# Performance work log

Measured on AMD Instinct MI355X. Metric: run time of the kernel, lower is better.

Reference implementation:

```python
import jax, jax.numpy as jnp
import numpy as np

B, S, D, H = 16, 2048, 1024, 1024

def setup_inputs() -> dict:
    key = jax.random.key(0)
    k1, k2, k3 = jax.random.split(key, 3)
    X = jax.random.normal(k1, (B, S, D), dtype=jnp.float32)
    W = jax.random.normal(k2, (3 * H, D), dtype=jnp.float32) * (1.0 / np.sqrt(D))
    b = jax.random.normal(k3, (3 * H,), dtype=jnp.float32) * 0.01
    return {"X": X, "W": W, "b": b}

def forget_mult(z, f):
    # z, f: [B, S, H]; h_t = z_t * f_t + (1 - f_t) * h_{t-1}, h_{-1} = 0
    z_t = jnp.moveaxis(z, 1, 0)  # [S, B, H]
    f_t = jnp.moveaxis(f, 1, 0)
    h0 = jnp.zeros(z.shape[::2], dtype=z.dtype)  # [B, H]
    def step(h, zf):
        zt, ft = zf
        h = zt * ft + (1.0 - ft) * h
        return h, h
    _, cs = jax.lax.scan(step, h0, (z_t, f_t))
    return jnp.moveaxis(cs, 0, 1)  # [B, S, H]

def reference(X, W, b):
    # window=1, output_gate=True, batch_first=True, zoneout=0, hidden=None
    Y = jnp.einsum('bsd,ed->bse', X, W) + b  # [B, S, 3H]
    z_gate, f_gate, o_gate = jnp.split(Y, 3, axis=2)
    z_gate = jnp.tanh(z_gate)
    f_gate = jax.nn.sigmoid(f_gate)
    c_gate = forget_mult(z_gate, f_gate)
    output = jax.nn.sigmoid(o_gate) * c_gate
    return output, c_gate[:, -1:]
```

## Files before the change

kernel.cpp:

```cpp
#include <hip/hip_runtime.h>
#include <hip/hip_bf16.h>
#include <hip/hip_fp16.h>


#define BB 16
#define SS 2048
#define DD 1024
#define HH 1024
#define N3 3072
#define CHUNK 64
#define NC (SS/CHUNK)

#define BM 256
#define BN 256
#define BK 64
#define NKT (DD/BK)

typedef _Float16 f16x8 __attribute__((ext_vector_type(8)));
typedef float    f32x4 __attribute__((ext_vector_type(4)));

__device__ __forceinline__ float sigm_f(float x) {
    return 1.0f / (1.0f + __expf(-x));
}
__device__ __forceinline__ float tanh_f(float x) {
    float ax = fabsf(x);
    float e  = __expf(2.0f * ax);
    float r  = 1.0f - 2.0f / (e + 1.0f);
    return copysignf(r, x);
}

__global__ __launch_bounds__(256) void cvt_f32_f16(
    const float* __restrict__ src, __half* __restrict__ dst, int n8)
{
    int i = blockIdx.x * 256 + threadIdx.x;
    if (i >= n8) return;
    const float4* s = (const float4*)src + (size_t)i * 2;
    float4 a = s[0], b = s[1];
    f16x8 v;
    v[0] = (_Float16)a.x; v[1] = (_Float16)a.y; v[2] = (_Float16)a.z; v[3] = (_Float16)a.w;
    v[4] = (_Float16)b.x; v[5] = (_Float16)b.y; v[6] = (_Float16)b.z; v[7] = (_Float16)b.w;
    *((f16x8*)dst + i) = v;
}

__global__ __launch_bounds__(512) void gemm_gates8(
    const __half* __restrict__ Xs,
    const __half* __restrict__ W16,
    const float*  __restrict__ bias,
    __half* __restrict__ G)
{
    __shared__ __half As[2][BM * BK] __attribute__((aligned(16)));
    __shared__ __half Bs[2][BN * BK] __attribute__((aligned(16)));

    const int t   = threadIdx.x;
    const int wid = t >> 6;
    const int l   = t & 63;
    const int m0  = blockIdx.x * BM;
    const int n0  = blockIdx.y * BN;
    const int wr  = wid >> 2;
    const int wc  = wid & 3;
    const int cl  = l & 15;
    const int kg  = l >> 4;
    const int cs  = cl & 7;

    f32x4 acc[8][4];
    #pragma unroll
    for (int m = 0; m < 8; ++m)
        #pragma unroll
        for (int n = 0; n < 4; ++n)
            acc[m][n] = f32x4{0.f, 0.f, 0.f, 0.f};

    const int srow = wid * 8 + (l >> 3);
    const int scol = (((l & 7) ^ ((l >> 3) & 7)) * 8);
    const __half* Xb = Xs  + (size_t)(m0 + srow) * DD + scol;
    const __half* Wb = W16 + (size_t)(n0 + srow) * DD + scol;

#define ISSUE_A(slot, j, kt) \
    __builtin_amdgcn_global_load_lds( \
        (const __attribute__((address_space(1))) void*)(Xb + (size_t)(j) * 64 * DD + (kt) * BK), \
        (__attribute__((address_space(3))) void*)(&As[slot][(j) * 4096 + wid * 512]), 16, 0, 0)
#define ISSUE_B(slot, j, kt) \
    __builtin_amdgcn_global_load_lds( \
        (const __attribute__((address_space(1))) void*)(Wb + (size_t)(j) * 64 * DD + (kt) * BK), \
        (__attribute__((address_space(3))) void*)(&Bs[slot][(j) * 4096 + wid * 512]), 16, 0, 0)

#define READ_A(rh) \
    _Pragma("unroll") \
    for (int i = 0; i < 4; ++i) \
        _Pragma("unroll") \
        for (int kh = 0; kh < 2; ++kh) \
            a[i][kh] = *(const f16x8*)(Ab + ((wr * 128 + ((rh) * 4 + i) * 16 + cl) * BK \
                                             + (((kh * 4 + kg) ^ cs) * 8)))
#define READ_B(bd, ch) \
    _Pragma("unroll") \
    for (int j = 0; j < 2; ++j) \
        _Pragma("unroll") \
        for (int kh = 0; kh < 2; ++kh) \
            bd[j][kh] = *(const f16x8*)(Bb + ((wc * 64 + ((ch) * 2 + j) * 16 + cl) * BK \
                                              + (((kh * 4 + kg) ^ cs) * 8)))

#define MFMA_Q(rh, ch, bd) \
    __builtin_amdgcn_s_barrier(); \
    asm volatile("s_waitcnt lgkmcnt(0)" ::: "memory"); \
    __builtin_amdgcn_sched_barrier(0); \
    __builtin_amdgcn_s_setprio(1); \
    _Pragma("unroll") \
    for (int kh = 0; kh < 2; ++kh) \
        _Pragma("unroll") \
        for (int i = 0; i < 4; ++i) \
            _Pragma("unroll") \
            for (int j = 0; j < 2; ++j) \
                acc[(rh) * 4 + i][(ch) * 2 + j] = __builtin_amdgcn_mfma_f32_16x16x32_f16( \
                    a[i][kh], bd[j][kh], acc[(rh) * 4 + i][(ch) * 2 + j], 0, 0, 0); \
    __builtin_amdgcn_s_setprio(0); \
    __builtin_amdgcn_sched_barrier(0); \
    __builtin_amdgcn_s_barrier()

    ISSUE_A(0, 0, 0); ISSUE_A(0, 1, 0); ISSUE_A(0, 2, 0); ISSUE_A(0, 3, 0);
    ISSUE_B(0, 0, 0); ISSUE_B(0, 1, 0); ISSUE_B(0, 2, 0); ISSUE_B(0, 3, 0);

    for (int kt = 0; kt < NKT; ++kt) {
        const int cur = kt & 1, nxt = cur ^ 1;
        const __half* Ab = As[cur];
        const __half* Bb = Bs[cur];

        if (kt + 1 < NKT) {
            ISSUE_A(nxt, 0, kt + 1); ISSUE_A(nxt, 1, kt + 1);
            ISSUE_A(nxt, 2, kt + 1); ISSUE_A(nxt, 3, kt + 1);
            asm volatile("s_waitcnt vmcnt(4)" ::: "memory");
        } else {
            asm volatile("s_waitcnt vmcnt(0)" ::: "memory");
        }
        __builtin_amdgcn_s_barrier();

        f16x8 a[4][2], b0[2][2], b1[2][2];

        READ_A(0); READ_B(b0, 0);
        MFMA_Q(0, 0, b0);

        READ_B(b1, 1);
        if (kt + 1 < NKT) {
            ISSUE_B(nxt, 0, kt + 1); ISSUE_B(nxt, 1, kt + 1);
            ISSUE_B(nxt, 2, kt + 1); ISSUE_B(nxt, 3, kt + 1);
        }
        MFMA_Q(0, 1, b1);

        READ_A(1);
        MFMA_Q(1, 1, b1);

        MFMA_Q(1, 0, b0);
    }
#undef MFMA_Q
#undef READ_A
#undef READ_B
#undef ISSUE_A
#undef ISSUE_B

    #pragma unroll
    for (int fc = 0; fc < 4; ++fc) {
        const int gcol = n0 + wc * 64 + fc * 16 + cl;
        const float bv = bias[gcol];
        #pragma unroll
        for (int fr = 0; fr < 8; ++fr) {
            const int grow0 = m0 + wr * 128 + fr * 16 + kg * 4;
            #pragma unroll
            for (int i = 0; i < 4; ++i) {
                G[(size_t)(grow0 + i) * N3 + gcol] = __float2half(acc[fr][fc][i] + bv);
            }
        }
    }
}

__global__ __launch_bounds__(256) void scan_pass1(
    const __half* __restrict__ G,
    float* __restrict__ Ac, float* __restrict__ Fc)
{
    const int flat = blockIdx.x * 256 + threadIdx.x;
    const int h  = flat & (HH - 1);
    const int c  = (flat >> 10) & (NC - 1);
    const int lb = flat >> 15;

    const __half* g = G + (size_t)(lb * SS + c * CHUNK) * N3 + h;
    float A = 0.f, F = 1.f;
    for (int s = 0; s < CHUNK; ++s) {
        float z = __half2float(g[0]);
        float f = __half2float(g[HH]);
        g += N3;
        float ft = sigm_f(f);
        float fp = 1.f - ft;
        A = tanh_f(z) * ft + fp * A;
        F *= fp;
    }
    Ac[flat] = A;
    Fc[flat] = F;
}

__global__ __launch_bounds__(256) void scan_pass2(
    const float* __restrict__ Ac, const float* __restrict__ Fc,
    float* __restrict__ Hin, float* __restrict__ c_last)
{
    const int flat = blockIdx.x * 256 + threadIdx.x;
    const int lb = flat >> 10;
    const int h  = flat & (HH - 1);
    float hc = 0.f;
    for (int c = 0; c < NC; ++c) {
        const size_t idx = (size_t)(lb * NC + c) * HH + h;
        Hin[idx] = hc;
        hc = Ac[idx] + Fc[idx] * hc;
    }
    c_last[flat] = hc;
}

__global__ __launch_bounds__(256) void scan_pass3(
    const __half* __restrict__ G, const float* __restrict__ Hin,
    float* __restrict__ out)
{
    const int flat = blockIdx.x * 256 + threadIdx.x;
    const int h  = flat & (HH - 1);
    const int c  = (flat >> 10) & (NC - 1);
    const int lb = flat >> 15;

    const __half* g = G + (size_t)(lb * SS + c * CHUNK) * N3 + h;
    float* o = out + (size_t)(lb * SS + c * CHUNK) * HH + h;
    float hc = Hin[flat];
    for (int s = 0; s < CHUNK; ++s) {
        float z  = __half2float(g[0]);
        float f  = __half2float(g[HH]);
        float og = __half2float(g[2 * HH]);
        g += N3;
        float ft = sigm_f(f);
        hc = tanh_f(z) * ft + (1.f - ft) * hc;
        *o = hc * sigm_f(og);
        o += HH;
    }
}

extern "C" void kernel_launch(void* const* d_in, const int* in_sizes, int n_in,
                              void* d_out, int out_size, void* d_ws, size_t ws_size,
                              hipStream_t stream) {
    const float* X    = (const float*)d_in[0];
    const float* W    = (const float*)d_in[1];
    const float* bias = (const float*)d_in[2];
    for (int i = 0; i < n_in && i < 3; ++i) {
        if      (in_sizes[i] == BB * SS * DD) X    = (const float*)d_in[i];
        else if (in_sizes[i] == N3 * DD)      W    = (const float*)d_in[i];
        else if (in_sizes[i] == N3)           bias = (const float*)d_in[i];
    }
    float* out = (float*)d_out;
    float* c_last_base = out + (size_t)BB * SS * HH;

    const size_t w16_b   = (size_t)N3 * DD * sizeof(__half);
    const size_t per_b_x = (size_t)SS * DD * sizeof(__half);
    const size_t per_b_g = (size_t)SS * N3 * sizeof(__half);
    const size_t per_b_s = (size_t)NC * HH * sizeof(float) * 3;
    int nb = 1;
    for (int cand = BB; cand >= 1; --cand) {
        if (w16_b + (size_t)cand * (per_b_x + per_b_g + per_b_s) <= ws_size) {
            nb = cand; break;
        }
    }

    __half* W16 = (__half*)d_ws;
    __half* X16 = (__half*)((char*)W16 + w16_b);
    __half* G   = (__half*)((char*)X16 + (size_t)nb * per_b_x);
    float*  Ac  = (float*)((char*)G + (size_t)nb * per_b_g);
    float*  Fc  = Ac + (size_t)nb * NC * HH;
    float*  Hin = Fc + (size_t)nb * NC * HH;

    {
        const int n8 = (N3 * DD) / 8;
        cvt_f32_f16<<<(n8 + 255) / 256, 256, 0, stream>>>(W, W16, n8);
    }

    for (int b0 = 0; b0 < BB; b0 += nb) {
        const int bs = (b0 + nb <= BB) ? nb : (BB - b0);

        const int n8x = (bs * SS * DD) / 8;
        cvt_f32_f16<<<(n8x + 255) / 256, 256, 0, stream>>>(
            X + (size_t)b0 * SS * DD, X16, n8x);

        dim3 gg(bs * (SS / BM), N3 / BN);
        gemm_gates8<<<gg, 512, 0, stream>>>(X16, W16, bias, G);

        scan_pass1<<<(bs * NC * HH) / 256, 256, 0, stream>>>(G, Ac, Fc);
        scan_pass2<<<(bs * HH) / 256, 256, 0, stream>>>(Ac, Fc, Hin,
                                                        c_last_base + (size_t)b0 * HH);
        scan_pass3<<<(bs * NC * HH) / 256, 256, 0, stream>>>(G, Hin,
                                                             out + (size_t)b0 * SS * HH);
    }
}
```

Measured before the change: 484.6 us.

## Stage GEMM epilogue through LDS for coalesced stores and trim barriers

Removes the two s_barriers around each MFMA quarter, leaving one barrier per k-iteration. The GEMM epilogue now writes the fp16 accumulators into shared memory in 64-row slabs, then each thread stores contiguous 16-byte vectors to G instead of scattered 2-byte writes. The batch chunk size is also capped at 8, presumably to keep the working set cache-resident. The extra LDS round-trips and barriers add epilogue cost, and dropping the barriers relies on the lgkmcnt waits to keep LDS reads ordered.

```diff
diff --git a/kernel.cpp b/kernel.cpp
--- a/kernel.cpp
+++ b/kernel.cpp
@@ -98,8 +98,7 @@
             bd[j][kh] = *(const f16x8*)(Bb + ((wc * 64 + ((ch) * 2 + j) * 16 + cl) * BK \
                                               + (((kh * 4 + kg) ^ cs) * 8)))
 
-#define MFMA_Q(rh, ch, bd) \
-    __builtin_amdgcn_s_barrier(); \
+#define WAIT_MFMA(rh, ch, bd) \
     asm volatile("s_waitcnt lgkmcnt(0)" ::: "memory"); \
     __builtin_amdgcn_sched_barrier(0); \
     __builtin_amdgcn_s_setprio(1); \
@@ -111,9 +110,7 @@
             for (int j = 0; j < 2; ++j) \
                 acc[(rh) * 4 + i][(ch) * 2 + j] = __builtin_amdgcn_mfma_f32_16x16x32_f16( \
                     a[i][kh], bd[j][kh], acc[(rh) * 4 + i][(ch) * 2 + j], 0, 0, 0); \
-    __builtin_amdgcn_s_setprio(0); \
-    __builtin_amdgcn_sched_barrier(0); \
-    __builtin_amdgcn_s_barrier()
+    __builtin_amdgcn_s_setprio(0)
 
     ISSUE_A(0, 0, 0); ISSUE_A(0, 1, 0); ISSUE_A(0, 2, 0); ISSUE_A(0, 3, 0);
     ISSUE_B(0, 0, 0); ISSUE_B(0, 1, 0); ISSUE_B(0, 2, 0); ISSUE_B(0, 3, 0);
@@ -135,38 +132,62 @@
         f16x8 a[4][2], b0[2][2], b1[2][2];
 
         READ_A(0); READ_B(b0, 0);
-        MFMA_Q(0, 0, b0);
+        WAIT_MFMA(0, 0, b0);
 
         READ_B(b1, 1);
         if (kt + 1 < NKT) {
             ISSUE_B(nxt, 0, kt + 1); ISSUE_B(nxt, 1, kt + 1);
             ISSUE_B(nxt, 2, kt + 1); ISSUE_B(nxt, 3, kt + 1);
         }
-        MFMA_Q(0, 1, b1);
+        WAIT_MFMA(0, 1, b1);
 
         READ_A(1);
-        MFMA_Q(1, 1, b1);
-
-        MFMA_Q(1, 0, b0);
-    }
-#undef MFMA_Q
+        WAIT_MFMA(1, 1, b1);
+
+        WAIT_MFMA(1, 0, b0);
+
+        __builtin_amdgcn_s_barrier();
+    }
+#undef WAIT_MFMA
 #undef READ_A
 #undef READ_B
 #undef ISSUE_A
 #undef ISSUE_B
 
+    __half* sh = &As[0][0];
+    const int bcol0 = n0 + wc * 64 + cl;
+    float bv[4];
     #pragma unroll
-    for (int fc = 0; fc < 4; ++fc) {
-        const int gcol = n0 + wc * 64 + fc * 16 + cl;
-        const float bv = bias[gcol];
-        #pragma unroll
-        for (int fr = 0; fr < 8; ++fr) {
-            const int grow0 = m0 + wr * 128 + fr * 16 + kg * 4;
+    for (int fc = 0; fc < 4; ++fc) bv[fc] = bias[bcol0 + fc * 16];
+
+    const int row_l = t >> 3;
+    const int chunk = t & 7;
+
+    #pragma unroll
+    for (int r = 0; r < 4; ++r) {
+        if (wr == (r >> 1)) {
             #pragma unroll
-            for (int i = 0; i < 4; ++i) {
-                G[(size_t)(grow0 + i) * N3 + gcol] = __float2half(acc[fr][fc][i] + bv);
+            for (int f4 = 0; f4 < 4; ++f4) {
+                const int fr = (r & 1) * 4 + f4;
+                #pragma unroll
+                for (int fc = 0; fc < 4; ++fc) {
+                    #pragma unroll
+                    for (int i = 0; i < 4; ++i) {
+                        sh[(f4 * 16 + kg * 4 + i) * 264 + wc * 64 + fc * 16 + cl] =
+                            __float2half(acc[fr][fc][i] + bv[fc]);
+                    }
+                }
             }
         }
+        __builtin_amdgcn_s_barrier();
+        {
+            const __half* src = sh + row_l * 264 + chunk * 32;
+            __half* dst = G + (size_t)(m0 + r * 64 + row_l) * N3 + n0 + chunk * 32;
+            #pragma unroll
+            for (int k = 0; k < 4; ++k)
+                *(f16x8*)(dst + k * 8) = *(const f16x8*)(src + k * 8);
+        }
+        __builtin_amdgcn_s_barrier();
     }
 }
 
@@ -258,6 +279,7 @@
             nb = cand; break;
         }
     }
+    if (nb > 8) nb = 8;
 
     __half* W16 = (__half*)d_ws;
     __half* X16 = (__half*)((char*)W16 + w16_b);
```

Measured after the change: 414.9 us (median of 4 runs). 14.4% less time.
